# Kernel tuning notes

Hardware: AMD Instinct MI355X
Metric: run time of the kernel (lower is better)

Reference implementation:

```python
import jax, jax.numpy as jnp
import numpy as np

EPS = 1e-5

def _conv(x, w, pad):
    # x: [B,C,H,W] NCHW, w: [O,I,kh,kw] OIHW
    return jax.lax.conv_general_dilated(
        x, w, (1, 1), [(pad, pad), (pad, pad)],
        dimension_numbers=('NCHW', 'OIHW', 'NCHW'))

def _bn(x, g, b, m, v):
    # eval-mode batchnorm folded into scale/shift
    s = g * jax.lax.rsqrt(v + EPS)
    return x * s[None, :, None, None] + (b - m * s)[None, :, None, None]

def _cbr(x, w, g, b, m, v):
    # Convolution block from CornerNet: conv3x3(pad=1, no bias) + BN + ReLU
    return jax.nn.relu(_bn(_conv(x, w, 1), g, b, m, v))


def setup_inputs() -> dict:
    key = jax.random.key(0)
    B, Cin, C, H, W = 4, 256, 256, 128, 128
    kdims = {'up': (C, Cin, 3, 3), 'down': (C, Cin, 3, 3),
             'p': (C, C, 3, 3), 'c1': (C, Cin, 1, 1), 'c2': (C, C, 3, 3)}
    inp = {'x': jax.random.normal(key, (B, Cin, H, W), dtype=jnp.float32)}
    for i, n in enumerate(['up', 'down', 'p', 'c1', 'c2']):
        ks = jax.random.split(jax.random.fold_in(key, i + 1), 5)
        inp['w_' + n] = jax.random.normal(ks[0], kdims[n], dtype=jnp.float32) * 0.02
        inp['g_' + n] = 1.0 + 0.1 * jax.random.normal(ks[1], (C,), dtype=jnp.float32)
        inp['b_' + n] = 0.1 * jax.random.normal(ks[2], (C,), dtype=jnp.float32)
        inp['m_' + n] = 0.1 * jax.random.normal(ks[3], (C,), dtype=jnp.float32)
        inp['v_' + n] = 0.5 + jax.random.uniform(ks[4], (C,), dtype=jnp.float32)
    return inp


def reference(x,
              w_up, g_up, b_up, m_up, v_up,
              w_down, g_down, b_down, m_down, v_down,
              w_p, g_p, b_p, m_p, v_p,
              w_c1, g_c1, b_c1, m_c1, v_c1,
              w_c2, g_c2, b_c2, m_c2, v_c2):
    # up branch: conv-bn-relu then LeftPool (reverse cummax over W) then RightPool (cummax over W)
    up = _cbr(x, w_up, g_up, b_up, m_up, v_up)
    up = jax.lax.cummax(up, axis=3, reverse=True)   # LeftPool
    up = jax.lax.cummax(up, axis=3)                 # RightPool
    # down branch: conv-bn-relu then TopPool (reverse cummax over H) then BottomPool (cummax over H)
    down = _cbr(x, w_down, g_down, b_down, m_down, v_down)
    down = jax.lax.cummax(down, axis=2, reverse=True)  # TopPool
    down = jax.lax.cummax(down, axis=2)                # BottomPool
    # merge path: 3x3 conv + BN on pooled sum
    merge = _bn(_conv(up + down, w_p, 1), g_p, b_p, m_p, v_p)
    # shortcut path: 1x1 conv + BN on input
    bn1 = _bn(_conv(x, w_c1, 0), g_c1, b_c1, m_c1, v_c1)
    relu1 = jax.nn.relu(merge + bn1)
    # output Convolution block
    return _cbr(relu1, w_c2, g_c2, b_c2, m_c2, v_c2)
```

## Files before the change

kernel.cpp:

```cpp
#include <hip/hip_runtime.h>

typedef unsigned short u16;
typedef __attribute__((ext_vector_type(8))) short bf16x8;
typedef __attribute__((ext_vector_type(4))) float f32x4;


__device__ __forceinline__ u16 f2bf(float f) {
  unsigned u = __float_as_uint(f);
  unsigned r = u + 0x7fffu + ((u >> 16) & 1u);
  return (u16)(r >> 16);
}

__device__ __forceinline__ void gll16(const char* g, char* l) {
  __builtin_amdgcn_global_load_lds((const __attribute__((address_space(1))) void*)g,
                                   (__attribute__((address_space(3))) void*)l, 16, 0, 0);
}

__global__ void bn_prep_kernel(const float* __restrict__ g, const float* __restrict__ b,
                               const float* __restrict__ m, const float* __restrict__ v,
                               float* __restrict__ st) {
  int c = threadIdx.x;
  float s = g[c] * rsqrtf(v[c] + 1e-5f);
  st[c] = s;
  st[256 + c] = b[c] - m[c] * s;
}

__global__ void bn_fix_kernel(float* __restrict__ st) {
  int c = threadIdx.x;
  st[2 * 512 + 256 + c] += st[3 * 512 + 256 + c];
  st[3 * 512 + c] = st[3 * 512 + c] / st[2 * 512 + c];
}

__global__ void wprep3_kernel(const float* __restrict__ w, u16* __restrict__ dst) {
  int idx = blockIdx.x * 256 + threadIdx.x;
  int blk = idx >> 12, iu = idx & 4095;
  int co_l = iu >> 5, w32 = iu & 31, slot = w32 >> 3, e = w32 & 7;
  int q = slot ^ ((co_l >> 1) & 3);
  int cohalf = blk / 72, step = blk % 72;
  int outer = step / 12, rr = step % 12, dwi = rr >> 2, kc = rr & 3;
  int half = outer / 3, d = outer % 3;
  int s = d * 3 + dwi;
  int ci = half * 128 + kc * 32 + q * 8 + e;
  int co = cohalf * 128 + co_l;
  dst[idx] = f2bf(w[(co * 256 + ci) * 9 + s]);
}

__global__ void wprep1_kernel(const float* __restrict__ w, u16* __restrict__ dst,
                              const float* __restrict__ ratio) {
  int idx = blockIdx.x * 256 + threadIdx.x;
  int blk = idx >> 12, iu = idx & 4095;
  int co_l = iu >> 5, w32 = iu & 31, slot = w32 >> 3, e = w32 & 7;
  int q = slot ^ ((co_l >> 1) & 3);
  int cohalf = blk >> 3, j = blk & 7;
  int half2 = j >> 2, kc = j & 3;
  int ci = half2 * 128 + kc * 32 + q * 8 + e;
  int co = cohalf * 128 + co_l;
  dst[idx] = f2bf(w[co * 256 + ci] * ratio[co]);
}

__global__ __launch_bounds__(256) void nchw_to_nhwc_kernel(const float* __restrict__ x,
                                                           char* __restrict__ xb) {
  __shared__ __align__(16) u16 tl[128 * 130];
  int bh = blockIdx.x; int b = bh >> 7, h = bh & 127;
  int t = threadIdx.x;
  for (int half = 0; half < 2; ++half) {
    __syncthreads();
    for (int i = 0; i < 64; ++i) {
      int cil = i * 2 + (t >> 7);
      int ci = half * 128 + cil;
      int w = t & 127;
      tl[w * 130 + cil] = f2bf(x[(size_t)((b * 256 + ci) * 128 + h) * 128 + w]);
    }
    __syncthreads();
    char* plane = xb + (size_t)(b * 128 + h) * 65536 + half * 32768;
    for (int i = 0; i < 32; ++i) {
      int w = i * 4 + (t >> 6);
      int c2 = (t & 63) * 2;
      unsigned v = *(const unsigned*)&tl[w * 130 + c2];
      *(unsigned*)(plane + w * 256 + ((c2 * 2) ^ (((w + 1) & 7) << 4))) = v;
    }
  }
}

__device__ __forceinline__ void stage_a(const char* wA1, const char* wA2, int step,
                                        char* ldsA0, int buf, int t) {
  const char* src = (step < 72) ? (wA1 + (size_t)step * 8192)
                                : (wA2 + (size_t)(step - 72) * 8192);
  char* dst = ldsA0 + buf * 8192 + t * 16;
  const char* g = src + t * 16;
  gll16(g, dst);
  gll16(g + 4096, dst + 4096);
}

__device__ __forceinline__ void stage_b(const char* plane, char* ldsB, int t) {
  if (plane) {
    char* dst = ldsB + 256 + t * 16;
    const char* g = plane + t * 16;
#pragma unroll
    for (int r = 0; r < 8; ++r) gll16(g + r * 4096, dst + r * 4096);
  } else {
    int4 z = {0, 0, 0, 0};
#pragma unroll
    for (int r = 0; r < 8; ++r) *(int4*)(ldsB + 256 + r * 4096 + t * 16) = z;
  }
}

__device__ __forceinline__ void conv_pipeline(const char* inB1, const char* inB2,
                                              const char* wA1, const char* wA2,
                                              int h, int nsteps, char* lds,
                                              f32x4 (&acc)[4][4]) {
  const int t = threadIdx.x;
  const int wv = t >> 6, lane = t & 63;
  const int lane15 = lane & 15, q = lane >> 4;
  const int coq = wv >> 1, wh = wv & 1;
  char* ldsB = lds;
  char* ldsA0 = lds + 33280;

  int aOff[4];
#pragma unroll
  for (int f = 0; f < 4; ++f) {
    int ra = coq * 64 + f * 16 + lane15;
    aOff[f] = ra * 64 + ((q ^ ((ra >> 1) & 3)) << 4);
  }
  int wpb[4];
#pragma unroll
  for (int f = 0; f < 4; ++f) wpb[f] = wh * 64 + f * 16 + lane15;

  {
    int4 z = {0, 0, 0, 0};
    if (t < 16) *(int4*)(ldsB + t * 16) = z;
    else if (t < 32) *(int4*)(ldsB + 33024 + (t - 16) * 16) = z;
  }

  int cur = 0, i = 0;
  for (int outer = 0; outer < 6; ++outer) {
    const int half = (outer >= 3) ? 1 : 0;
    const int d = outer - half * 3;
    const int hs = h + d - 1;
    const char* plane = (hs >= 0 && hs < 128)
                            ? inB1 + (size_t)hs * 65536 + (size_t)half * 32768
                            : nullptr;
    stage_b(plane, ldsB, t);
    if (outer == 0) stage_a(wA1, wA2, 0, ldsA0, 0, t);
    __syncthreads();
#pragma unroll
    for (int dwi = 0; dwi < 3; ++dwi)
#pragma unroll
      for (int kc = 0; kc < 4; ++kc) {
        if (i + 1 < nsteps) stage_a(wA1, wA2, i + 1, ldsA0, cur ^ 1, t);
        bf16x8 af[4], bf[4];
        const char* lA = ldsA0 + cur * 8192;
#pragma unroll
        for (int f = 0; f < 4; ++f) af[f] = *(const bf16x8*)(lA + aOff[f]);
#pragma unroll
        for (int f = 0; f < 4; ++f) {
          int wp = wpb[f] + dwi;
          bf[f] = *(const bf16x8*)(ldsB + wp * 256 + ((kc * 64 + q * 16) ^ ((wp & 7) << 4)));
        }
#pragma unroll
        for (int fm = 0; fm < 4; ++fm)
#pragma unroll
          for (int fn = 0; fn < 4; ++fn)
            acc[fm][fn] = __builtin_amdgcn_mfma_f32_16x16x32_bf16(af[fm], bf[fn], acc[fm][fn], 0, 0, 0);
        __syncthreads();
        cur ^= 1;
        ++i;
      }
  }
  if (nsteps > 72) {
    for (int half2 = 0; half2 < 2; ++half2) {
      stage_b(inB2 + (size_t)h * 65536 + (size_t)half2 * 32768, ldsB, t);
      __syncthreads();
#pragma unroll
      for (int kc = 0; kc < 4; ++kc) {
        if (i + 1 < nsteps) stage_a(wA1, wA2, i + 1, ldsA0, cur ^ 1, t);
        bf16x8 af[4], bf[4];
        const char* lA = ldsA0 + cur * 8192;
#pragma unroll
        for (int f = 0; f < 4; ++f) af[f] = *(const bf16x8*)(lA + aOff[f]);
#pragma unroll
        for (int f = 0; f < 4; ++f) {
          int wp = wpb[f] + 1;
          bf[f] = *(const bf16x8*)(ldsB + wp * 256 + ((kc * 64 + q * 16) ^ ((wp & 7) << 4)));
        }
#pragma unroll
        for (int fm = 0; fm < 4; ++fm)
#pragma unroll
          for (int fn = 0; fn < 4; ++fn)
            acc[fm][fn] = __builtin_amdgcn_mfma_f32_16x16x32_bf16(af[fm], bf[fn], acc[fm][fn], 0, 0, 0);
        __syncthreads();
        cur ^= 1;
        ++i;
      }
    }
  }
}

__device__ __forceinline__ void zero_acc(f32x4 (&acc)[4][4]) {
  f32x4 z = {0.f, 0.f, 0.f, 0.f};
#pragma unroll
  for (int i = 0; i < 4; ++i)
#pragma unroll
    for (int j = 0; j < 4; ++j) acc[i][j] = z;
}

__device__ __forceinline__ void store_pad_relu(f32x4 (&acc)[4][4], const float* __restrict__ st,
                                               int cohalf, int b, int h, char* __restrict__ out) {
  const int t = threadIdx.x, lane = t & 63, wv = t >> 6;
  const int lane15 = lane & 15, q = lane >> 4, coq = wv >> 1, wh = wv & 1;
  char* plane = out + (size_t)(b * 128 + h) * 65536 + cohalf * 32768;
#pragma unroll
  for (int fm = 0; fm < 4; ++fm) {
    int co_l = coq * 64 + fm * 16 + q * 4;
    int co = cohalf * 128 + co_l;
    float ss[4], tt[4];
#pragma unroll
    for (int r = 0; r < 4; ++r) { ss[r] = st[co + r]; tt[r] = st[256 + co + r]; }
#pragma unroll
    for (int fn = 0; fn < 4; ++fn) {
      int w = wh * 64 + fn * 16 + lane15;
      short4 o;
      o.x = (short)f2bf(fmaxf(acc[fm][fn][0] * ss[0] + tt[0], 0.f));
      o.y = (short)f2bf(fmaxf(acc[fm][fn][1] * ss[1] + tt[1], 0.f));
      o.z = (short)f2bf(fmaxf(acc[fm][fn][2] * ss[2] + tt[2], 0.f));
      o.w = (short)f2bf(fmaxf(acc[fm][fn][3] * ss[3] + tt[3], 0.f));
      *(short4*)(plane + w * 256 + ((co_l * 2) ^ (((w + 1) & 7) << 4))) = o;
    }
  }
}

__global__ __launch_bounds__(256, 3) void conv_up_kernel(const char* __restrict__ xb,
                                                         const char* __restrict__ wp,
                                                         const float* __restrict__ st,
                                                         float* __restrict__ rmax) {
  __shared__ __align__(16) char lds[49664];
  int swz = (blockIdx.x & 7) * 64 + (blockIdx.x >> 3);
  int b = swz >> 7, h = swz & 127;
  int cohalf = blockIdx.y;
  f32x4 acc[4][4];
  zero_acc(acc);
  conv_pipeline(xb + (size_t)b * 8388608, nullptr, wp + (size_t)cohalf * 589824, nullptr,
                h, 72, lds, acc);

  const int t = threadIdx.x, lane = t & 63, wv = t >> 6;
  const int lane15 = lane & 15, q = lane >> 4, coq = wv >> 1, wh = wv & 1;
  float* rlds = (float*)lds;
  __syncthreads();
#pragma unroll
  for (int fm = 0; fm < 4; ++fm) {
    int co_l = coq * 64 + fm * 16 + q * 4;
    int co = cohalf * 128 + co_l;
#pragma unroll
    for (int r = 0; r < 4; ++r) {
      float ss = st[co + r], tt = st[256 + co + r];
      float v = 0.f;
#pragma unroll
      for (int fn = 0; fn < 4; ++fn) v = fmaxf(v, acc[fm][fn][r] * ss + tt);
      v = fmaxf(v, __shfl_xor(v, 1));
      v = fmaxf(v, __shfl_xor(v, 2));
      v = fmaxf(v, __shfl_xor(v, 4));
      v = fmaxf(v, __shfl_xor(v, 8));
      if (lane15 == 0) rlds[wh * 128 + co_l + r] = v;
    }
  }
  __syncthreads();
  if (t < 128)
    rmax[(size_t)(b * 128 + h) * 256 + cohalf * 128 + t] = fmaxf(rlds[t], rlds[128 + t]);
}

__global__ __launch_bounds__(256, 3) void conv_down_kernel(const char* __restrict__ xb,
                                                           const char* __restrict__ wp,
                                                           const float* __restrict__ st,
                                                           char* __restrict__ out) {
  __shared__ __align__(16) char lds[49664];
  int swz = (blockIdx.x & 7) * 64 + (blockIdx.x >> 3);
  int b = swz >> 7, h = swz & 127;
  int cohalf = blockIdx.y;
  f32x4 acc[4][4];
  zero_acc(acc);
  conv_pipeline(xb + (size_t)b * 8388608, nullptr, wp + (size_t)cohalf * 589824, nullptr,
                h, 72, lds, acc);
  store_pad_relu(acc, st, cohalf, b, h, out);
}

__global__ __launch_bounds__(256) void colmax_kernel(const char* __restrict__ dp,
                                                     float* __restrict__ cmax) {
  int bw = blockIdx.x; int b = bw >> 7, w = bw & 127;
  int c = threadIdx.x;
  size_t base = (size_t)b * 8388608 + (size_t)(c >> 7) * 32768 + w * 256 +
                (((c & 127) * 2) ^ (((w + 1) & 7) << 4));
  float m = 0.f;
  for (int h = 0; h < 128; ++h) {
    u16 raw = *(const u16*)(dp + base + (size_t)h * 65536);
    m = fmaxf(m, __uint_as_float(((unsigned)raw) << 16));
  }
  cmax[(size_t)(b * 128 + w) * 256 + c] = m;
}

__global__ __launch_bounds__(256) void pooled_kernel(const float* __restrict__ rmax,
                                                     const float* __restrict__ cmax,
                                                     char* __restrict__ dp) {
  int bh = blockIdx.x; int b = bh >> 7, h = bh & 127;
  int c = threadIdx.x;
  float rm = rmax[(size_t)(b * 128 + h) * 256 + c];
  char* plane = dp + (size_t)(b * 128 + h) * 65536 + (c >> 7) * 32768;
  int cb = (c & 127) * 2;
  for (int w = 0; w < 128; ++w) {
    float v = rm + cmax[(size_t)(b * 128 + w) * 256 + c];
    *(u16*)(plane + w * 256 + (cb ^ (((w + 1) & 7) << 4))) = f2bf(v);
  }
}

__global__ __launch_bounds__(256, 3) void conv_merge_kernel(const char* __restrict__ dp,
                                                            const char* __restrict__ xb,
                                                            const char* __restrict__ wp_p,
                                                            const char* __restrict__ wp_c1,
                                                            const float* __restrict__ st,
                                                            char* __restrict__ out) {
  __shared__ __align__(16) char lds[49664];
  int swz = (blockIdx.x & 7) * 64 + (blockIdx.x >> 3);
  int b = swz >> 7, h = swz & 127;
  int cohalf = blockIdx.y;
  f32x4 acc[4][4];
  zero_acc(acc);
  conv_pipeline(dp + (size_t)b * 8388608, xb + (size_t)b * 8388608,
                wp_p + (size_t)cohalf * 589824, wp_c1 + (size_t)cohalf * 65536,
                h, 80, lds, acc);
  store_pad_relu(acc, st, cohalf, b, h, out);
}

__global__ __launch_bounds__(256, 3) void conv_c2_kernel(const char* __restrict__ relu1,
                                                         const char* __restrict__ wp,
                                                         const float* __restrict__ st,
                                                         float* __restrict__ out) {
  __shared__ __align__(16) char lds[49664];
  int swz = (blockIdx.x & 7) * 64 + (blockIdx.x >> 3);
  int b = swz >> 7, h = swz & 127;
  int cohalf = blockIdx.y;
  f32x4 acc[4][4];
  zero_acc(acc);
  conv_pipeline(relu1 + (size_t)b * 8388608, nullptr, wp + (size_t)cohalf * 589824, nullptr,
                h, 72, lds, acc);

  const int t = threadIdx.x, lane = t & 63, wv = t >> 6;
  const int lane15 = lane & 15, q = lane >> 4, coq = wv >> 1, wh = wv & 1;
  float* tl = (float*)lds;
  for (int g = 0; g < 8; ++g) {
    __syncthreads();
    if (coq == (g >> 2)) {
      int fm = g & 3;
      int co_l = coq * 64 + fm * 16 + q * 4;
      int co = cohalf * 128 + co_l;
#pragma unroll
      for (int r = 0; r < 4; ++r) {
        float ss = st[co + r], tt = st[256 + co + r];
#pragma unroll
        for (int fn = 0; fn < 4; ++fn) {
          int w = wh * 64 + fn * 16 + lane15;
          tl[(q * 4 + r) * 132 + w] = fmaxf(acc[fm][fn][r] * ss + tt, 0.f);
        }
      }
    }
    __syncthreads();
    int row = t >> 4, ch = t & 15;
    int co = cohalf * 128 + g * 16 + row;
    float* dst = out + (size_t)((b * 256 + co) * 128 + h) * 128 + ch * 8;
    float4 p0 = *(float4*)&tl[row * 132 + ch * 8];
    float4 p1 = *(float4*)&tl[row * 132 + ch * 8 + 4];
    *(float4*)dst = p0;
    *(float4*)(dst + 4) = p1;
  }
}

extern "C" void kernel_launch(void* const* d_in, const int* in_sizes, int n_in,
                              void* d_out, int out_size, void* d_ws, size_t ws_size,
                              hipStream_t stream) {
  (void)in_sizes; (void)n_in; (void)out_size; (void)ws_size;
  const float* x    = (const float*)d_in[0];
  const float* w_up = (const float*)d_in[1];
  const float* w_dn = (const float*)d_in[6];
  const float* w_p  = (const float*)d_in[11];
  const float* w_c1 = (const float*)d_in[16];
  const float* w_c2 = (const float*)d_in[21];

  char* ws = (char*)d_ws;
  char* xb    = ws;
  char* dp    = ws + 33554432ull;
  char* relu1 = ws + 67108864ull;
  u16* wp_up  = (u16*)(ws + 100663296ull);
  u16* wp_dn  = (u16*)(ws + 101842944ull);
  u16* wp_p   = (u16*)(ws + 103022592ull);
  u16* wp_c2  = (u16*)(ws + 104202240ull);
  u16* wp_c1  = (u16*)(ws + 105381888ull);
  float* st   = (float*)(ws + 105512960ull);
  float* rmax = (float*)(ws + 105523200ull);
  float* cmax = (float*)(ws + 106047488ull);

  bn_prep_kernel<<<1, 256, 0, stream>>>((const float*)d_in[2], (const float*)d_in[3],
                                        (const float*)d_in[4], (const float*)d_in[5], st);
  bn_prep_kernel<<<1, 256, 0, stream>>>((const float*)d_in[7], (const float*)d_in[8],
                                        (const float*)d_in[9], (const float*)d_in[10], st + 512);
  bn_prep_kernel<<<1, 256, 0, stream>>>((const float*)d_in[12], (const float*)d_in[13],
                                        (const float*)d_in[14], (const float*)d_in[15], st + 1024);
  bn_prep_kernel<<<1, 256, 0, stream>>>((const float*)d_in[17], (const float*)d_in[18],
                                        (const float*)d_in[19], (const float*)d_in[20], st + 1536);
  bn_prep_kernel<<<1, 256, 0, stream>>>((const float*)d_in[22], (const float*)d_in[23],
                                        (const float*)d_in[24], (const float*)d_in[25], st + 2048);
  bn_fix_kernel<<<1, 256, 0, stream>>>(st);

  wprep3_kernel<<<2304, 256, 0, stream>>>(w_up, wp_up);
  wprep3_kernel<<<2304, 256, 0, stream>>>(w_dn, wp_dn);
  wprep3_kernel<<<2304, 256, 0, stream>>>(w_p, wp_p);
  wprep3_kernel<<<2304, 256, 0, stream>>>(w_c2, wp_c2);
  wprep1_kernel<<<256, 256, 0, stream>>>(w_c1, wp_c1, st + 1536);

  nchw_to_nhwc_kernel<<<512, 256, 0, stream>>>(x, xb);

  conv_up_kernel<<<dim3(512, 2), 256, 0, stream>>>(xb, (const char*)wp_up, st, rmax);
  conv_down_kernel<<<dim3(512, 2), 256, 0, stream>>>(xb, (const char*)wp_dn, st + 512, dp);
  colmax_kernel<<<512, 256, 0, stream>>>(dp, cmax);
  pooled_kernel<<<512, 256, 0, stream>>>(rmax, cmax, dp);
  conv_merge_kernel<<<dim3(512, 2), 256, 0, stream>>>(dp, xb, (const char*)wp_p,
                                                      (const char*)wp_c1, st + 1024, relu1);
  conv_c2_kernel<<<dim3(512, 2), 256, 0, stream>>>(relu1, (const char*)wp_c2, st + 2048,
                                                   (float*)d_out);
}
```

Before: 397.6 us.

## Load weight fragments directly from global into registers, dropping LDS staging and per-step barriers

Weights are repacked so each lane's MFMA A-fragment is a contiguous 16-byte chunk. Each wave now loads its fragments straight from global memory into registers, double-buffered one step ahead, instead of staging them through LDS. This removes the LDS A buffers and the __syncthreads after every k-step, keeping barriers only per input-row plane, and shrinks LDS to 33280 bytes. The trade-off is more global/L2 traffic, since the two waves sharing a coq slice both fetch the same weights, plus more registers held live for the prefetch.

```diff
diff --git a/kernel.cpp b/kernel.cpp
--- a/kernel.cpp
+++ b/kernel.cpp
@@ -33,28 +33,26 @@
 
 __global__ void wprep3_kernel(const float* __restrict__ w, u16* __restrict__ dst) {
   int idx = blockIdx.x * 256 + threadIdx.x;
-  int blk = idx >> 12, iu = idx & 4095;
-  int co_l = iu >> 5, w32 = iu & 31, slot = w32 >> 3, e = w32 & 7;
-  int q = slot ^ ((co_l >> 1) & 3);
+  int e = idx & 7, lane = (idx >> 3) & 63, f = (idx >> 9) & 3, coq = (idx >> 11) & 1;
+  int blk = idx >> 12;
   int cohalf = blk / 72, step = blk % 72;
   int outer = step / 12, rr = step % 12, dwi = rr >> 2, kc = rr & 3;
   int half = outer / 3, d = outer % 3;
   int s = d * 3 + dwi;
-  int ci = half * 128 + kc * 32 + q * 8 + e;
-  int co = cohalf * 128 + co_l;
+  int co = cohalf * 128 + coq * 64 + f * 16 + (lane & 15);
+  int ci = half * 128 + kc * 32 + (lane >> 4) * 8 + e;
   dst[idx] = f2bf(w[(co * 256 + ci) * 9 + s]);
 }
 
 __global__ void wprep1_kernel(const float* __restrict__ w, u16* __restrict__ dst,
                               const float* __restrict__ ratio) {
   int idx = blockIdx.x * 256 + threadIdx.x;
-  int blk = idx >> 12, iu = idx & 4095;
-  int co_l = iu >> 5, w32 = iu & 31, slot = w32 >> 3, e = w32 & 7;
-  int q = slot ^ ((co_l >> 1) & 3);
-  int cohalf = blk >> 3, j = blk & 7;
-  int half2 = j >> 2, kc = j & 3;
-  int ci = half2 * 128 + kc * 32 + q * 8 + e;
-  int co = cohalf * 128 + co_l;
+  int e = idx & 7, lane = (idx >> 3) & 63, f = (idx >> 9) & 3, coq = (idx >> 11) & 1;
+  int blk = idx >> 12;
+  int cohalf = blk >> 3, step = blk & 7;
+  int half2 = step >> 2, kc = step & 3;
+  int co = cohalf * 128 + coq * 64 + f * 16 + (lane & 15);
+  int ci = half2 * 128 + kc * 32 + (lane >> 4) * 8 + e;
   dst[idx] = f2bf(w[co * 256 + ci] * ratio[co]);
 }
 
@@ -82,16 +80,6 @@
   }
 }
 
-__device__ __forceinline__ void stage_a(const char* wA1, const char* wA2, int step,
-                                        char* ldsA0, int buf, int t) {
-  const char* src = (step < 72) ? (wA1 + (size_t)step * 8192)
-                                : (wA2 + (size_t)(step - 72) * 8192);
-  char* dst = ldsA0 + buf * 8192 + t * 16;
-  const char* g = src + t * 16;
-  gll16(g, dst);
-  gll16(g + 4096, dst + 4096);
-}
-
 __device__ __forceinline__ void stage_b(const char* plane, char* ldsB, int t) {
   if (plane) {
     char* dst = ldsB + 256 + t * 16;
@@ -103,6 +91,13 @@
 #pragma unroll
     for (int r = 0; r < 8; ++r) *(int4*)(ldsB + 256 + r * 4096 + t * 16) = z;
   }
+}
+
+__device__ __forceinline__ const char* a_src(const char* wA1, const char* wA2, int step,
+                                             int coq, int lane) {
+  const char* src = (step < 72) ? (wA1 + (size_t)step * 8192)
+                                : (wA2 + (size_t)(step - 72) * 8192);
+  return src + coq * 4096 + lane * 16;
 }
 
 __device__ __forceinline__ void conv_pipeline(const char* inB1, const char* inB2,
@@ -114,14 +109,7 @@
   const int lane15 = lane & 15, q = lane >> 4;
   const int coq = wv >> 1, wh = wv & 1;
   char* ldsB = lds;
-  char* ldsA0 = lds + 33280;
-
-  int aOff[4];
-#pragma unroll
-  for (int f = 0; f < 4; ++f) {
-    int ra = coq * 64 + f * 16 + lane15;
-    aOff[f] = ra * 64 + ((q ^ ((ra >> 1) & 3)) << 4);
-  }
+
   int wpb[4];
 #pragma unroll
   for (int f = 0; f < 4; ++f) wpb[f] = wh * 64 + f * 16 + lane15;
@@ -132,7 +120,14 @@
     else if (t < 32) *(int4*)(ldsB + 33024 + (t - 16) * 16) = z;
   }
 
-  int cur = 0, i = 0;
+  bf16x8 aCur[4], aNxt[4];
+  {
+    const char* p = a_src(wA1, wA2, 0, coq, lane);
+#pragma unroll
+    for (int f = 0; f < 4; ++f) aCur[f] = *(const bf16x8*)(p + f * 1024);
+  }
+
+  int i = 0;
   for (int outer = 0; outer < 6; ++outer) {
     const int half = (outer >= 3) ? 1 : 0;
     const int d = outer - half * 3;
@@ -141,17 +136,16 @@
                             ? inB1 + (size_t)hs * 65536 + (size_t)half * 32768
                             : nullptr;
     stage_b(plane, ldsB, t);
-    if (outer == 0) stage_a(wA1, wA2, 0, ldsA0, 0, t);
     __syncthreads();
 #pragma unroll
     for (int dwi = 0; dwi < 3; ++dwi)
 #pragma unroll
       for (int kc = 0; kc < 4; ++kc) {
-        if (i + 1 < nsteps) stage_a(wA1, wA2, i + 1, ldsA0, cur ^ 1, t);
-        bf16x8 af[4], bf[4];
-        const char* lA = ldsA0 + cur * 8192;
-#pragma unroll
-        for (int f = 0; f < 4; ++f) af[f] = *(const bf16x8*)(lA + aOff[f]);
+        int ns = (i + 1 < nsteps) ? i + 1 : 0;
+        const char* p = a_src(wA1, wA2, ns, coq, lane);
+#pragma unroll
+        for (int f = 0; f < 4; ++f) aNxt[f] = *(const bf16x8*)(p + f * 1024);
+        bf16x8 bf[4];
 #pragma unroll
         for (int f = 0; f < 4; ++f) {
           int wp = wpb[f] + dwi;
@@ -161,11 +155,12 @@
         for (int fm = 0; fm < 4; ++fm)
 #pragma unroll
           for (int fn = 0; fn < 4; ++fn)
-            acc[fm][fn] = __builtin_amdgcn_mfma_f32_16x16x32_bf16(af[fm], bf[fn], acc[fm][fn], 0, 0, 0);
-        __syncthreads();
-        cur ^= 1;
+            acc[fm][fn] = __builtin_amdgcn_mfma_f32_16x16x32_bf16(aCur[fm], bf[fn], acc[fm][fn], 0, 0, 0);
+#pragma unroll
+        for (int f = 0; f < 4; ++f) aCur[f] = aNxt[f];
         ++i;
       }
+    __syncthreads();
   }
   if (nsteps > 72) {
     for (int half2 = 0; half2 < 2; ++half2) {
@@ -173,11 +168,11 @@
       __syncthreads();
 #pragma unroll
       for (int kc = 0; kc < 4; ++kc) {
-        if (i + 1 < nsteps) stage_a(wA1, wA2, i + 1, ldsA0, cur ^ 1, t);
-        bf16x8 af[4], bf[4];
-        const char* lA = ldsA0 + cur * 8192;
-#pragma unroll
-        for (int f = 0; f < 4; ++f) af[f] = *(const bf16x8*)(lA + aOff[f]);
+        int ns = (i + 1 < nsteps) ? i + 1 : 0;
+        const char* p = a_src(wA1, wA2, ns, coq, lane);
+#pragma unroll
+        for (int f = 0; f < 4; ++f) aNxt[f] = *(const bf16x8*)(p + f * 1024);
+        bf16x8 bf[4];
 #pragma unroll
         for (int f = 0; f < 4; ++f) {
           int wp = wpb[f] + 1;
@@ -187,11 +182,12 @@
         for (int fm = 0; fm < 4; ++fm)
 #pragma unroll
           for (int fn = 0; fn < 4; ++fn)
-            acc[fm][fn] = __builtin_amdgcn_mfma_f32_16x16x32_bf16(af[fm], bf[fn], acc[fm][fn], 0, 0, 0);
-        __syncthreads();
-        cur ^= 1;
+            acc[fm][fn] = __builtin_amdgcn_mfma_f32_16x16x32_bf16(aCur[fm], bf[fn], acc[fm][fn], 0, 0, 0);
+#pragma unroll
+        for (int f = 0; f < 4; ++f) aCur[f] = aNxt[f];
         ++i;
       }
+      __syncthreads();
     }
   }
 }
@@ -233,14 +229,14 @@
                                                          const char* __restrict__ wp,
                                                          const float* __restrict__ st,
                                                          float* __restrict__ rmax) {
-  __shared__ __align__(16) char lds[49664];
+  __shared__ __align__(16) char lds[33280];
   int swz = (blockIdx.x & 7) * 64 + (blockIdx.x >> 3);
   int b = swz >> 7, h = swz & 127;
   int cohalf = blockIdx.y;
+  const char* wA = wp + (size_t)cohalf * 589824;
   f32x4 acc[4][4];
   zero_acc(acc);
-  conv_pipeline(xb + (size_t)b * 8388608, nullptr, wp + (size_t)cohalf * 589824, nullptr,
-                h, 72, lds, acc);
+  conv_pipeline(xb + (size_t)b * 8388608, nullptr, wA, wA, h, 72, lds, acc);
 
   const int t = threadIdx.x, lane = t & 63, wv = t >> 6;
   const int lane15 = lane & 15, q = lane >> 4, coq = wv >> 1, wh = wv & 1;
@@ -272,14 +268,14 @@
                                                            const char* __restrict__ wp,
                                                            const float* __restrict__ st,
                                                            char* __restrict__ out) {
-  __shared__ __align__(16) char lds[49664];
+  __shared__ __align__(16) char lds[33280];
   int swz = (blockIdx.x & 7) * 64 + (blockIdx.x >> 3);
   int b = swz >> 7, h = swz & 127;
   int cohalf = blockIdx.y;
+  const char* wA = wp + (size_t)cohalf * 589824;
   f32x4 acc[4][4];
   zero_acc(acc);
-  conv_pipeline(xb + (size_t)b * 8388608, nullptr, wp + (size_t)cohalf * 589824, nullptr,
-                h, 72, lds, acc);
+  conv_pipeline(xb + (size_t)b * 8388608, nullptr, wA, wA, h, 72, lds, acc);
   store_pad_relu(acc, st, cohalf, b, h, out);
 }
 
@@ -317,7 +313,7 @@
                                                             const char* __restrict__ wp_c1,
                                                             const float* __restrict__ st,
                                                             char* __restrict__ out) {
-  __shared__ __align__(16) char lds[49664];
+  __shared__ __align__(16) char lds[33280];
   int swz = (blockIdx.x & 7) * 64 + (blockIdx.x >> 3);
   int b = swz >> 7, h = swz & 127;
   int cohalf = blockIdx.y;
@@ -333,14 +329,14 @@
                                                          const char* __restrict__ wp,
                                                          const float* __restrict__ st,
                                                          float* __restrict__ out) {
-  __shared__ __align__(16) char lds[49664];
+  __shared__ __align__(16) char lds[33280];
   int swz = (blockIdx.x & 7) * 64 + (blockIdx.x >> 3);
   int b = swz >> 7, h = swz & 127;
   int cohalf = blockIdx.y;
+  const char* wA = wp + (size_t)cohalf * 589824;
   f32x4 acc[4][4];
   zero_acc(acc);
-  conv_pipeline(relu1 + (size_t)b * 8388608, nullptr, wp + (size_t)cohalf * 589824, nullptr,
-                h, 72, lds, acc);
+  conv_pipeline(relu1 + (size_t)b * 8388608, nullptr, wA, wA, h, 72, lds, acc);
 
   const int t = threadIdx.x, lane = t & 63, wv = t >> 6;
   const int lane15 = lane & 15, q = lane >> 4, coq = wv >> 1, wh = wv & 1;
@@ -387,11 +383,11 @@
   char* xb    = ws;
   char* dp    = ws + 33554432ull;
   char* relu1 = ws + 67108864ull;
-  u16* wp_up  = (u16*)(ws + 100663296ull);
-  u16* wp_dn  = (u16*)(ws + 101842944ull);
-  u16* wp_p   = (u16*)(ws + 103022592ull);
-  u16* wp_c2  = (u16*)(ws + 104202240ull);
-  u16* wp_c1  = (u16*)(ws + 105381888ull);
+  char* wp_up = ws + 100663296ull;
+  char* wp_dn = ws + 101842944ull;
+  char* wp_p  = ws + 103022592ull;
+  char* wp_c2 = ws + 104202240ull;
+  char* wp_c1 = ws + 105381888ull;
   float* st   = (float*)(ws + 105512960ull);
   float* rmax = (float*)(ws + 105523200ull);
   float* cmax = (float*)(ws + 106047488ull);
@@ -408,20 +404,18 @@
                                         (const float*)d_in[24], (const float*)d_in[25], st + 2048);
   bn_fix_kernel<<<1, 256, 0, stream>>>(st);
 
-  wprep3_kernel<<<2304, 256, 0, stream>>>(w_up, wp_up);
-  wprep3_kernel<<<2304, 256, 0, stream>>>(w_dn, wp_dn);
-  wprep3_kernel<<<2304, 256, 0, stream>>>(w_p, wp_p);
-  wprep3_kernel<<<2304, 256, 0, stream>>>(w_c2, wp_c2);
-  wprep1_kernel<<<256, 256, 0, stream>>>(w_c1, wp_c1, st + 1536);
+  wprep3_kernel<<<2304, 256, 0, stream>>>(w_up, (u16*)wp_up);
+  wprep3_kernel<<<2304, 256, 0, stream>>>(w_dn, (u16*)wp_dn);
+  wprep3_kernel<<<2304, 256, 0, stream>>>(w_p, (u16*)wp_p);
+  wprep3_kernel<<<2304, 256, 0, stream>>>(w_c2, (u16*)wp_c2);
+  wprep1_kernel<<<256, 256, 0, stream>>>(w_c1, (u16*)wp_c1, st + 1536);
 
   nchw_to_nhwc_kernel<<<512, 256, 0, stream>>>(x, xb);
 
-  conv_up_kernel<<<dim3(512, 2), 256, 0, stream>>>(xb, (const char*)wp_up, st, rmax);
-  conv_down_kernel<<<dim3(512, 2), 256, 0, stream>>>(xb, (const char*)wp_dn, st + 512, dp);
+  conv_up_kernel<<<dim3(512, 2), 256, 0, stream>>>(xb, wp_up, st, rmax);
+  conv_down_kernel<<<dim3(512, 2), 256, 0, stream>>>(xb, wp_dn, st + 512, dp);
   colmax_kernel<<<512, 256, 0, stream>>>(dp, cmax);
   pooled_kernel<<<512, 256, 0, stream>>>(rmax, cmax, dp);
-  conv_merge_kernel<<<dim3(512, 2), 256, 0, stream>>>(dp, xb, (const char*)wp_p,
-                                                      (const char*)wp_c1, st + 1024, relu1);
-  conv_c2_kernel<<<dim3(512, 2), 256, 0, stream>>>(relu1, (const char*)wp_c2, st + 2048,
-                                                   (float*)d_out);
-}
+  conv_merge_kernel<<<dim3(512, 2), 256, 0, stream>>>(dp, xb, wp_p, wp_c1, st + 1024, relu1);
+  conv_c2_kernel<<<dim3(512, 2), 256, 0, stream>>>(relu1, wp_c2, st + 2048, (float*)d_out);
+}
```

Result: slower. 460.4 us (+15.8%).

## Fuse up and down branch convolutions into one kernel sharing input tiles

Applied to the files above, without the earlier changes.

Merges the separate up and down 3x3 conv kernels into one kernel. Each staged input plane in LDS now feeds two accumulator sets, one per weight set, which halves input loads and launches. It also wraps the MFMA blocks in s_setprio to raise wave priority during matrix math. The trade-off is double the accumulator registers and more LDS, and the launch bounds no longer ask for 3 blocks per CU, so occupancy likely drops.

```diff
diff --git a/kernel.cpp b/kernel.cpp
--- a/kernel.cpp
+++ b/kernel.cpp
@@ -92,6 +92,13 @@
   gll16(g + 4096, dst + 4096);
 }
 
+__device__ __forceinline__ void stage_a72(const char* base, int step, char* ldsA0, int buf, int t) {
+  const char* g = base + (size_t)step * 8192 + t * 16;
+  char* dst = ldsA0 + buf * 8192 + t * 16;
+  gll16(g, dst);
+  gll16(g + 4096, dst + 4096);
+}
+
 __device__ __forceinline__ void stage_b(const char* plane, char* ldsB, int t) {
   if (plane) {
     char* dst = ldsB + 256 + t * 16;
@@ -102,6 +109,91 @@
     int4 z = {0, 0, 0, 0};
 #pragma unroll
     for (int r = 0; r < 8; ++r) *(int4*)(ldsB + 256 + r * 4096 + t * 16) = z;
+  }
+}
+
+__device__ __forceinline__ void zero_acc(f32x4 (&acc)[4][4]) {
+  f32x4 z = {0.f, 0.f, 0.f, 0.f};
+#pragma unroll
+  for (int i = 0; i < 4; ++i)
+#pragma unroll
+    for (int j = 0; j < 4; ++j) acc[i][j] = z;
+}
+
+__device__ __forceinline__ void conv_pipeline2(const char* inB, const char* wU, const char* wD,
+                                               int h, char* lds,
+                                               f32x4 (&accU)[4][4], f32x4 (&accD)[4][4]) {
+  const int t = threadIdx.x;
+  const int wv = t >> 6, lane = t & 63;
+  const int lane15 = lane & 15, q = lane >> 4;
+  const int coq = wv >> 1, wh = wv & 1;
+  char* ldsB = lds;
+  char* ldsAU = lds + 33280;
+  char* ldsAD = lds + 49664;
+
+  int aOff[4];
+#pragma unroll
+  for (int f = 0; f < 4; ++f) {
+    int ra = coq * 64 + f * 16 + lane15;
+    aOff[f] = ra * 64 + ((q ^ ((ra >> 1) & 3)) << 4);
+  }
+  int wpb[4];
+#pragma unroll
+  for (int f = 0; f < 4; ++f) wpb[f] = wh * 64 + f * 16 + lane15;
+
+  {
+    int4 z = {0, 0, 0, 0};
+    if (t < 16) *(int4*)(ldsB + t * 16) = z;
+    else if (t < 32) *(int4*)(ldsB + 33024 + (t - 16) * 16) = z;
+  }
+
+  int cur = 0, i = 0;
+  for (int outer = 0; outer < 6; ++outer) {
+    const int half = (outer >= 3) ? 1 : 0;
+    const int d = outer - half * 3;
+    const int hs = h + d - 1;
+    const char* plane = (hs >= 0 && hs < 128)
+                            ? inB + (size_t)hs * 65536 + (size_t)half * 32768
+                            : nullptr;
+    stage_b(plane, ldsB, t);
+    if (outer == 0) {
+      stage_a72(wU, 0, ldsAU, 0, t);
+      stage_a72(wD, 0, ldsAD, 0, t);
+    }
+    __syncthreads();
+#pragma unroll
+    for (int dwi = 0; dwi < 3; ++dwi)
+#pragma unroll
+      for (int kc = 0; kc < 4; ++kc) {
+        if (i + 1 < 72) {
+          stage_a72(wU, i + 1, ldsAU, cur ^ 1, t);
+          stage_a72(wD, i + 1, ldsAD, cur ^ 1, t);
+        }
+        bf16x8 aU[4], aD[4], bf[4];
+        const char* lAU = ldsAU + cur * 8192;
+        const char* lAD = ldsAD + cur * 8192;
+#pragma unroll
+        for (int f = 0; f < 4; ++f) aU[f] = *(const bf16x8*)(lAU + aOff[f]);
+#pragma unroll
+        for (int f = 0; f < 4; ++f) aD[f] = *(const bf16x8*)(lAD + aOff[f]);
+#pragma unroll
+        for (int f = 0; f < 4; ++f) {
+          int wp = wpb[f] + dwi;
+          bf[f] = *(const bf16x8*)(ldsB + wp * 256 + ((kc * 64 + q * 16) ^ ((wp & 7) << 4)));
+        }
+        __builtin_amdgcn_s_setprio(1);
+#pragma unroll
+        for (int fm = 0; fm < 4; ++fm)
+#pragma unroll
+          for (int fn = 0; fn < 4; ++fn) {
+            accU[fm][fn] = __builtin_amdgcn_mfma_f32_16x16x32_bf16(aU[fm], bf[fn], accU[fm][fn], 0, 0, 0);
+            accD[fm][fn] = __builtin_amdgcn_mfma_f32_16x16x32_bf16(aD[fm], bf[fn], accD[fm][fn], 0, 0, 0);
+          }
+        __builtin_amdgcn_s_setprio(0);
+        __syncthreads();
+        cur ^= 1;
+        ++i;
+      }
   }
 }
 
@@ -157,11 +249,13 @@
           int wp = wpb[f] + dwi;
           bf[f] = *(const bf16x8*)(ldsB + wp * 256 + ((kc * 64 + q * 16) ^ ((wp & 7) << 4)));
         }
+        __builtin_amdgcn_s_setprio(1);
 #pragma unroll
         for (int fm = 0; fm < 4; ++fm)
 #pragma unroll
           for (int fn = 0; fn < 4; ++fn)
             acc[fm][fn] = __builtin_amdgcn_mfma_f32_16x16x32_bf16(af[fm], bf[fn], acc[fm][fn], 0, 0, 0);
+        __builtin_amdgcn_s_setprio(0);
         __syncthreads();
         cur ^= 1;
         ++i;
@@ -183,25 +277,19 @@
           int wp = wpb[f] + 1;
           bf[f] = *(const bf16x8*)(ldsB + wp * 256 + ((kc * 64 + q * 16) ^ ((wp & 7) << 4)));
         }
+        __builtin_amdgcn_s_setprio(1);
 #pragma unroll
         for (int fm = 0; fm < 4; ++fm)
 #pragma unroll
           for (int fn = 0; fn < 4; ++fn)
             acc[fm][fn] = __builtin_amdgcn_mfma_f32_16x16x32_bf16(af[fm], bf[fn], acc[fm][fn], 0, 0, 0);
+        __builtin_amdgcn_s_setprio(0);
         __syncthreads();
         cur ^= 1;
         ++i;
       }
     }
   }
-}
-
-__device__ __forceinline__ void zero_acc(f32x4 (&acc)[4][4]) {
-  f32x4 z = {0.f, 0.f, 0.f, 0.f};
-#pragma unroll
-  for (int i = 0; i < 4; ++i)
-#pragma unroll
-    for (int j = 0; j < 4; ++j) acc[i][j] = z;
 }
 
 __device__ __forceinline__ void store_pad_relu(f32x4 (&acc)[4][4], const float* __restrict__ st,
@@ -229,21 +317,27 @@
   }
 }
 
-__global__ __launch_bounds__(256, 3) void conv_up_kernel(const char* __restrict__ xb,
-                                                         const char* __restrict__ wp,
-                                                         const float* __restrict__ st,
-                                                         float* __restrict__ rmax) {
-  __shared__ __align__(16) char lds[49664];
+__global__ __launch_bounds__(256) void conv_updown_kernel(const char* __restrict__ xb,
+                                                          const char* __restrict__ wp_u,
+                                                          const char* __restrict__ wp_d,
+                                                          const float* __restrict__ st,
+                                                          float* __restrict__ rmax,
+                                                          char* __restrict__ dn_out) {
+  __shared__ __align__(16) char lds[66048];
   int swz = (blockIdx.x & 7) * 64 + (blockIdx.x >> 3);
   int b = swz >> 7, h = swz & 127;
   int cohalf = blockIdx.y;
-  f32x4 acc[4][4];
-  zero_acc(acc);
-  conv_pipeline(xb + (size_t)b * 8388608, nullptr, wp + (size_t)cohalf * 589824, nullptr,
-                h, 72, lds, acc);
+  f32x4 accU[4][4], accD[4][4];
+  zero_acc(accU);
+  zero_acc(accD);
+  conv_pipeline2(xb + (size_t)b * 8388608, wp_u + (size_t)cohalf * 589824,
+                 wp_d + (size_t)cohalf * 589824, h, lds, accU, accD);
 
   const int t = threadIdx.x, lane = t & 63, wv = t >> 6;
   const int lane15 = lane & 15, q = lane >> 4, coq = wv >> 1, wh = wv & 1;
+  const float* stU = st;
+  const float* stD = st + 512;
+  store_pad_relu(accD, stD, cohalf, b, h, dn_out);
   float* rlds = (float*)lds;
   __syncthreads();
 #pragma unroll
@@ -252,10 +346,10 @@
     int co = cohalf * 128 + co_l;
 #pragma unroll
     for (int r = 0; r < 4; ++r) {
-      float ss = st[co + r], tt = st[256 + co + r];
+      float ss = stU[co + r], tt = stU[256 + co + r];
       float v = 0.f;
 #pragma unroll
-      for (int fn = 0; fn < 4; ++fn) v = fmaxf(v, acc[fm][fn][r] * ss + tt);
+      for (int fn = 0; fn < 4; ++fn) v = fmaxf(v, accU[fm][fn][r] * ss + tt);
       v = fmaxf(v, __shfl_xor(v, 1));
       v = fmaxf(v, __shfl_xor(v, 2));
       v = fmaxf(v, __shfl_xor(v, 4));
@@ -266,21 +360,6 @@
   __syncthreads();
   if (t < 128)
     rmax[(size_t)(b * 128 + h) * 256 + cohalf * 128 + t] = fmaxf(rlds[t], rlds[128 + t]);
-}
-
-__global__ __launch_bounds__(256, 3) void conv_down_kernel(const char* __restrict__ xb,
-                                                           const char* __restrict__ wp,
-                                                           const float* __restrict__ st,
-                                                           char* __restrict__ out) {
-  __shared__ __align__(16) char lds[49664];
-  int swz = (blockIdx.x & 7) * 64 + (blockIdx.x >> 3);
-  int b = swz >> 7, h = swz & 127;
-  int cohalf = blockIdx.y;
-  f32x4 acc[4][4];
-  zero_acc(acc);
-  conv_pipeline(xb + (size_t)b * 8388608, nullptr, wp + (size_t)cohalf * 589824, nullptr,
-                h, 72, lds, acc);
-  store_pad_relu(acc, st, cohalf, b, h, out);
 }
 
 __global__ __launch_bounds__(256) void colmax_kernel(const char* __restrict__ dp,
@@ -337,10 +416,10 @@
   int swz = (blockIdx.x & 7) * 64 + (blockIdx.x >> 3);
   int b = swz >> 7, h = swz & 127;
   int cohalf = blockIdx.y;
+  const char* wA = wp + (size_t)cohalf * 589824;
   f32x4 acc[4][4];
   zero_acc(acc);
-  conv_pipeline(relu1 + (size_t)b * 8388608, nullptr, wp + (size_t)cohalf * 589824, nullptr,
-                h, 72, lds, acc);
+  conv_pipeline(relu1 + (size_t)b * 8388608, nullptr, wA, wA, h, 72, lds, acc);
 
   const int t = threadIdx.x, lane = t & 63, wv = t >> 6;
   const int lane15 = lane & 15, q = lane >> 4, coq = wv >> 1, wh = wv & 1;
@@ -387,11 +466,11 @@
   char* xb    = ws;
   char* dp    = ws + 33554432ull;
   char* relu1 = ws + 67108864ull;
-  u16* wp_up  = (u16*)(ws + 100663296ull);
-  u16* wp_dn  = (u16*)(ws + 101842944ull);
-  u16* wp_p   = (u16*)(ws + 103022592ull);
-  u16* wp_c2  = (u16*)(ws + 104202240ull);
-  u16* wp_c1  = (u16*)(ws + 105381888ull);
+  char* wp_up = ws + 100663296ull;
+  char* wp_dn = ws + 101842944ull;
+  char* wp_p  = ws + 103022592ull;
+  char* wp_c2 = ws + 104202240ull;
+  char* wp_c1 = ws + 105381888ull;
   float* st   = (float*)(ws + 105512960ull);
   float* rmax = (float*)(ws + 105523200ull);
   float* cmax = (float*)(ws + 106047488ull);
@@ -408,20 +487,17 @@
                                         (const float*)d_in[24], (const float*)d_in[25], st + 2048);
   bn_fix_kernel<<<1, 256, 0, stream>>>(st);
 
-  wprep3_kernel<<<2304, 256, 0, stream>>>(w_up, wp_up);
-  wprep3_kernel<<<2304, 256, 0, stream>>>(w_dn, wp_dn);
-  wprep3_kernel<<<2304, 256, 0, stream>>>(w_p, wp_p);
-  wprep3_kernel<<<2304, 256, 0, stream>>>(w_c2, wp_c2);
-  wprep1_kernel<<<256, 256, 0, stream>>>(w_c1, wp_c1, st + 1536);
+  wprep3_kernel<<<2304, 256, 0, stream>>>(w_up, (u16*)wp_up);
+  wprep3_kernel<<<2304, 256, 0, stream>>>(w_dn, (u16*)wp_dn);
+  wprep3_kernel<<<2304, 256, 0, stream>>>(w_p, (u16*)wp_p);
+  wprep3_kernel<<<2304, 256, 0, stream>>>(w_c2, (u16*)wp_c2);
+  wprep1_kernel<<<256, 256, 0, stream>>>(w_c1, (u16*)wp_c1, st + 1536);
 
   nchw_to_nhwc_kernel<<<512, 256, 0, stream>>>(x, xb);
 
-  conv_up_kernel<<<dim3(512, 2), 256, 0, stream>>>(xb, (const char*)wp_up, st, rmax);
-  conv_down_kernel<<<dim3(512, 2), 256, 0, stream>>>(xb, (const char*)wp_dn, st + 512, dp);
+  conv_updown_kernel<<<dim3(512, 2), 256, 0, stream>>>(xb, wp_up, wp_dn, st, rmax, dp);
   colmax_kernel<<<512, 256, 0, stream>>>(dp, cmax);
   pooled_kernel<<<512, 256, 0, stream>>>(rmax, cmax, dp);
-  conv_merge_kernel<<<dim3(512, 2), 256, 0, stream>>>(dp, xb, (const char*)wp_p,
-                                                      (const char*)wp_c1, st + 1024, relu1);
-  conv_c2_kernel<<<dim3(512, 2), 256, 0, stream>>>(relu1, (const char*)wp_c2, st + 2048,
-                                                   (float*)d_out);
-}
+  conv_merge_kernel<<<dim3(512, 2), 256, 0, stream>>>(dp, xb, wp_p, wp_c1, st + 1024, relu1);
+  conv_c2_kernel<<<dim3(512, 2), 256, 0, stream>>>(relu1, wp_c2, st + 2048, (float*)d_out);
+}
```

After: 409.1 us. +2.9%, slower.
